# Performance work log

Measured on AMD Instinct MI355X. Metric: run time of the kernel, lower is better.

## Reference

```python
import jax, jax.numpy as jnp
import numpy as np

N = 50000   # num_nodes
R = 8       # num_relations
H = 128     # hidden_l
L = 32      # num_labels
E = 1600000 # num_edges


def setup_inputs() -> dict:
    key = jax.random.key(0)
    ks = jax.random.split(key, 8)
    edge_index = jax.random.randint(ks[0], (2, E), 0, N, dtype=jnp.int64)
    edge_type = jax.random.randint(ks[1], (E,), 0, R, dtype=jnp.int64)
    # layer 1: in_channels = num_nodes (x=None -> one-hot features)
    weight1 = jax.random.normal(ks[2], (R, N, H), dtype=jnp.float32) * 0.02
    root1 = jax.random.normal(ks[3], (N, H), dtype=jnp.float32) * 0.02
    bias1 = jnp.zeros((H,), dtype=jnp.float32)
    # layer 2: hidden -> labels
    weight2 = jax.random.normal(ks[4], (R, H, L), dtype=jnp.float32) * 0.05
    root2 = jax.random.normal(ks[5], (H, L), dtype=jnp.float32) * 0.05
    bias2 = jnp.zeros((L,), dtype=jnp.float32)
    return {"weight1": weight1, "root1": root1, "bias1": bias1,
            "weight2": weight2, "root2": root2, "bias2": bias2,
            "edge_index": edge_index, "edge_type": edge_type}


def _rel_mean_agg(msg, dst, et, num_nodes, num_rel):
    """PyG RGCNConv aggr='mean': mean over incoming edges per (node, relation),
    then sum over relations. msg: [E, F]."""
    seg = dst * num_rel + et  # combined (node, relation) segment id
    sums = jax.ops.segment_sum(msg, seg, num_segments=num_nodes * num_rel)
    cnt = jax.ops.segment_sum(jnp.ones((msg.shape[0],), msg.dtype), seg,
                              num_segments=num_nodes * num_rel)
    mean = sums / jnp.maximum(cnt, 1.0)[:, None]  # zero where count==0
    return mean.reshape(num_nodes, num_rel, -1).sum(axis=1)  # [N, F]


def reference(weight1, root1, bias1, weight2, root2, bias2, edge_index, edge_type):
    src, dst = edge_index[0], edge_index[1]
    # ---- layer 1 (x=None): message = weight1[r, src] row gather ----
    msg1 = weight1[edge_type, src]                      # [E, H]
    x = _rel_mean_agg(msg1, dst, edge_type, N, R) + root1 + bias1
    x = jax.nn.relu(x)
    # ---- layer 2: per-relation matmul then gather ----
    xw = jnp.einsum('nh,rhl->nrl', x, weight2)          # [N, R, L]
    msg2 = xw[src, edge_type]                           # [E, L]
    out = _rel_mean_agg(msg2, dst, edge_type, N, R) + x @ root2 + bias2
    return jax.nn.sigmoid(out)
```

## Files before the change

### kernel.cpp

```cpp
#include <hip/hip_runtime.h>
#include <math.h>

#define NN 50000
#define RR 8
#define HH 128
#define LL 32
#define EE 1600000
#define BW 128
#define NB 391
#define PB 782

#define FMA4(A, V, C) { A.x += (V).x*(C); A.y += (V).y*(C); A.z += (V).z*(C); A.w += (V).w*(C); }

typedef __attribute__((ext_vector_type(8))) short short8_t;
typedef __attribute__((ext_vector_type(4))) float f32x4_t;

__device__ __forceinline__ float bflo(unsigned u) { return __uint_as_float(u << 16); }
__device__ __forceinline__ float bfhi(unsigned u) { return __uint_as_float(u & 0xFFFF0000u); }
__device__ __forceinline__ unsigned bfpk(float a, float b) {
    unsigned ua = __float_as_uint(a), ub = __float_as_uint(b);
    ua = (ua + 0x7FFFu + ((ua >> 16) & 1u)) >> 16;
    ub = (ub + 0x7FFFu + ((ub >> 16) & 1u)) >> 16;
    return ua | (ub << 16);
}
__device__ __forceinline__ unsigned short bf16r(float f) {
    unsigned u = __float_as_uint(f);
    return (unsigned short)((u + 0x7FFFu + ((u >> 16) & 1u)) >> 16);
}

__global__ __launch_bounds__(256) void hist_kernel(const int* __restrict__ ei,
                                                   unsigned* __restrict__ ph) {
    __shared__ unsigned h[NB];
    int blk = blockIdx.x, tid = threadIdx.x;
    for (int i = tid; i < NB; i += 256) h[i] = 0;
    __syncthreads();
    int base = blk * 2048;
    if (blk < PB - 1) {
        const uint4* dp = (const uint4*)(ei + EE + base);
        uint4 d0 = dp[tid], d1 = dp[tid + 256];
        atomicAdd(&h[d0.x >> 7], 1u); atomicAdd(&h[d0.y >> 7], 1u);
        atomicAdd(&h[d0.z >> 7], 1u); atomicAdd(&h[d0.w >> 7], 1u);
        atomicAdd(&h[d1.x >> 7], 1u); atomicAdd(&h[d1.y >> 7], 1u);
        atomicAdd(&h[d1.z >> 7], 1u); atomicAdd(&h[d1.w >> 7], 1u);
    } else {
#pragma unroll
        for (int k = 0; k < 8; ++k) {
            int e = base + k * 256 + tid;
            if (e < EE) atomicAdd(&h[(unsigned)ei[EE + e] >> 7], 1u);
        }
    }
    __syncthreads();
    for (int i = tid; i < NB; i += 256) ph[blk * NB + i] = h[i];
}

__global__ __launch_bounds__(256) void bred_kernel(const unsigned* __restrict__ ph,
                                                   unsigned* __restrict__ pho,
                                                   unsigned* __restrict__ bcnt) {
    __shared__ unsigned s[256];
    int b = blockIdx.x, t = threadIdx.x;
    unsigned v[4];
    unsigned loc = 0;
#pragma unroll
    for (int j = 0; j < 4; ++j) {
        int idx = t * 4 + j;
        v[j] = (idx < PB) ? ph[(size_t)idx * NB + b] : 0;
        loc += v[j];
    }
    s[t] = loc;
    __syncthreads();
    for (int off = 1; off < 256; off <<= 1) {
        unsigned u = (t >= off) ? s[t - off] : 0; __syncthreads();
        if (t >= off) s[t] += u; __syncthreads();
    }
    unsigned run = (t > 0) ? s[t - 1] : 0;
#pragma unroll
    for (int j = 0; j < 4; ++j) {
        int idx = t * 4 + j;
        if (idx < PB) { unsigned c = v[j]; pho[(size_t)b * PB + idx] = run; run += c; }
    }
    if (t == 255) bcnt[b] = s[255];
}

__global__ __launch_bounds__(512) void bscan_kernel(const unsigned* __restrict__ bcnt,
                                                    unsigned* __restrict__ boff,
                                                    unsigned* __restrict__ node_off,
                                                    unsigned* __restrict__ srcr) {
    __shared__ unsigned s[512];
    int t = threadIdx.x;
    unsigned v = (t < NB) ? bcnt[t] : 0;
    s[t] = v; __syncthreads();
    for (int off = 1; off < 512; off <<= 1) {
        unsigned u = (t >= off) ? s[t - off] : 0; __syncthreads();
        if (t >= off) s[t] += u; __syncthreads();
    }
    if (t < NB) boff[t] = s[t] - v;
    if (t == 0) { boff[NB] = EE; node_off[NN] = EE; }
    if (t < 64) srcr[EE + t] = 0;
}

__global__ __launch_bounds__(256) void part_conv(const int* __restrict__ ei,
                                                 const int* __restrict__ et,
                                                 const unsigned* __restrict__ boff,
                                                 const unsigned* __restrict__ pho,
                                                 unsigned* __restrict__ tmp,
                                                 const float4* __restrict__ w1,
                                                 const float* __restrict__ w2,
                                                 uint4* __restrict__ w1b,
                                                 unsigned* __restrict__ wtb) {
    __shared__ unsigned h[NB];
    int b = blockIdx.x, tid = threadIdx.x;
    if (b >= PB) {
        if (b < PB + 25000) {
            size_t t = (size_t)(b - PB) * 256 + tid;
            float4 a = w1[2 * t], c = w1[2 * t + 1];
            uint4 o;
            o.x = bfpk(a.x, a.y); o.y = bfpk(a.z, a.w);
            o.z = bfpk(c.x, c.y); o.w = bfpk(c.z, c.w);
            w1b[t] = o;
        } else {
            int c = tid, r = c >> 5, l = c & 31;
            const float* wp = w2 + (size_t)r * HH * LL + l;
            for (int k = 0; k < HH; k += 2)
                wtb[c * 64 + (k >> 1)] = bfpk(wp[k * LL], wp[(k + 1) * LL]);
        }
        return;
    }
    for (int i = tid; i < NB; i += 256) h[i] = boff[i] + pho[(size_t)i * PB + b];
    __syncthreads();
    int base = b * 2048;
#pragma unroll
    for (int k = 0; k < 8; ++k) {
        int e = base + k * 256 + tid;
        if (e < EE) {
            unsigned sN = (unsigned)ei[e], d = (unsigned)ei[EE + e], r = (unsigned)et[e];
            unsigned p = atomicAdd(&h[d >> 7], 1u);
            tmp[p] = sN | (r << 16) | ((d & 127u) << 19);
        }
    }
}

__global__ __launch_bounds__(256) void finalize_kernel(const unsigned* __restrict__ boff,
                                                       const unsigned* __restrict__ tmp,
                                                       unsigned* __restrict__ node_off,
                                                       float* __restrict__ inv,
                                                       unsigned* __restrict__ srcr) {
    __shared__ unsigned cnt[BW * RR];
    __shared__ unsigned cur[BW];
    __shared__ unsigned excl[BW];
    int b = blockIdx.x, t = threadIdx.x;
    unsigned lo = boff[b], hi = boff[b + 1];
    int nn0 = b * BW;
    int nloc = NN - nn0 < BW ? NN - nn0 : BW;
    for (int i = t; i < BW * RR; i += 256) cnt[i] = 0;
    __syncthreads();
    for (unsigned i = lo + t; i < hi; i += 256) {
        unsigned v = tmp[i];
        atomicAdd(&cnt[((v >> 19) & 127u) * RR + ((v >> 16) & 7u)], 1u);
    }
    __syncthreads();
    unsigned own = 0;
    if (t < BW) {
#pragma unroll
        for (int r = 0; r < RR; ++r) own += cnt[t * RR + r];
        excl[t] = own;
    }
    __syncthreads();
    for (int off = 1; off < BW; off <<= 1) {
        unsigned u = 0;
        if (t < BW && t >= off) u = excl[t - off];
        __syncthreads();
        if (t < BW && t >= off) excl[t] += u;
        __syncthreads();
    }
    if (t < nloc) {
        unsigned o = lo + excl[t] - own;
        node_off[nn0 + t] = o;
        cur[t] = o;
    }
    __syncthreads();
    for (int i = t; i < nloc * RR; i += 256) {
        unsigned c = cnt[i];
        inv[(size_t)nn0 * RR + i] = c ? 1.f / (float)c : 0.f;
    }
    for (unsigned i = lo + t; i < hi; i += 256) {
        unsigned v = tmp[i];
        unsigned p = atomicAdd(&cur[(v >> 19) & 127u], 1u);
        srcr[p] = v & 0x7FFFFu;
    }
}

__global__ __launch_bounds__(256) void l1_gather(const unsigned* __restrict__ node_off,
                                                 const unsigned* __restrict__ srcr,
                                                 const float* __restrict__ inv,
                                                 const uint4* __restrict__ w1b,
                                                 const float* __restrict__ root1,
                                                 const float* __restrict__ bias1,
                                                 uint4* __restrict__ xb) {
    int wid = threadIdx.x >> 6, lane = threadIdx.x & 63;
    int n = blockIdx.x * 4 + wid;
    if (n >= NN) return;
    int q = lane >> 4, ql = lane & 15;
    int beg = node_off[n], end = node_off[n + 1];
    int cnt = end - beg;
    int nfull = cnt >> 4;
    float myinv = inv[n * RR + (lane & 7)];
    float4 a0 = {0.f, 0.f, 0.f, 0.f}, a1 = {0.f, 0.f, 0.f, 0.f};
    int e = beg + q;
    unsigned kp0 = srcr[e], kp1 = srcr[e + 4], kp2 = srcr[e + 8], kp3 = srcr[e + 12];
#define GATH(K, C) {                                                        \
        unsigned ss = (K) & 0xFFFFu, rr = (K) >> 16;                        \
        uint4 v = w1b[((size_t)rr * NN + ss) * 16 + ql];                    \
        a0.x = fmaf(bflo(v.x), (C), a0.x); a0.y = fmaf(bfhi(v.x), (C), a0.y); \
        a0.z = fmaf(bflo(v.y), (C), a0.z); a0.w = fmaf(bfhi(v.y), (C), a0.w); \
        a1.x = fmaf(bflo(v.z), (C), a1.x); a1.y = fmaf(bfhi(v.z), (C), a1.y); \
        a1.z = fmaf(bflo(v.w), (C), a1.z); a1.w = fmaf(bfhi(v.w), (C), a1.w); }
#pragma unroll 1
    for (int it = 0; it < nfull; ++it) {
        unsigned k0 = kp0, k1 = kp1, k2 = kp2, k3 = kp3;
        e += 16;
        kp0 = srcr[e]; kp1 = srcr[e + 4]; kp2 = srcr[e + 8]; kp3 = srcr[e + 12];
        float c0 = __shfl(myinv, (int)(k0 >> 16));
        float c1 = __shfl(myinv, (int)(k1 >> 16));
        float c2 = __shfl(myinv, (int)(k2 >> 16));
        float c3 = __shfl(myinv, (int)(k3 >> 16));
        GATH(k0, c0); GATH(k1, c1); GATH(k2, c2); GATH(k3, c3);
    }
    {
        float c0 = __shfl(myinv, (int)(kp0 >> 16));
        float c1 = __shfl(myinv, (int)(kp1 >> 16));
        float c2 = __shfl(myinv, (int)(kp2 >> 16));
        float c3 = __shfl(myinv, (int)(kp3 >> 16));
        if (e < end)      GATH(kp0, c0);
        if (e + 4 < end)  GATH(kp1, c1);
        if (e + 8 < end)  GATH(kp2, c2);
        if (e + 12 < end) GATH(kp3, c3);
    }
#undef GATH
#define RED(c) { c += __shfl_xor(c, 16); c += __shfl_xor(c, 32); }
    RED(a0.x); RED(a0.y); RED(a0.z); RED(a0.w);
    RED(a1.x); RED(a1.y); RED(a1.z); RED(a1.w);
#undef RED
    if (q == 0) {
        const float4* rt = (const float4*)(root1 + (size_t)n * HH);
        const float4* bs = (const float4*)bias1;
        float4 rA = rt[2 * ql], rB = rt[2 * ql + 1];
        float4 bA = bs[2 * ql], bB = bs[2 * ql + 1];
        float o0 = fmaxf(a0.x + rA.x + bA.x, 0.f);
        float o1 = fmaxf(a0.y + rA.y + bA.y, 0.f);
        float o2 = fmaxf(a0.z + rA.z + bA.z, 0.f);
        float o3 = fmaxf(a0.w + rA.w + bA.w, 0.f);
        float o4 = fmaxf(a1.x + rB.x + bB.x, 0.f);
        float o5 = fmaxf(a1.y + rB.y + bB.y, 0.f);
        float o6 = fmaxf(a1.z + rB.z + bB.z, 0.f);
        float o7 = fmaxf(a1.w + rB.w + bB.w, 0.f);
        uint4 o;
        o.x = bfpk(o0, o1); o.y = bfpk(o2, o3);
        o.z = bfpk(o4, o5); o.w = bfpk(o6, o7);
        xb[(size_t)n * 16 + ql] = o;
    }
}

__global__ __launch_bounds__(256) void xw_mfma(const unsigned* __restrict__ xb,
                                               const unsigned* __restrict__ wtb,
                                               unsigned short* __restrict__ xwb) {
    int tid = threadIdx.x, wid = tid >> 6, l = tid & 63;
    int bn = blockIdx.x >> 2;
    int bc = blockIdx.x & 3;
    int col = bc * 64 + wid * 16 + (l & 15);
    int kq = l >> 4;
    short8_t bfr[4];
    const unsigned* wcol = wtb + col * 64;
#pragma unroll
    for (int ks = 0; ks < 4; ++ks)
        bfr[ks] = *reinterpret_cast<const short8_t*>(wcol + ks * 16 + kq * 4);
    int n0 = bn * 64;
#pragma unroll
    for (int sub = 0; sub < 4; ++sub) {
        int row = n0 + sub * 16 + (l & 15);
        int rc = row < NN ? row : NN - 1;
        const unsigned* xr = xb + (size_t)rc * 64;
        f32x4_t acc = {0.f, 0.f, 0.f, 0.f};
#pragma unroll
        for (int ks = 0; ks < 4; ++ks) {
            short8_t a = *reinterpret_cast<const short8_t*>(xr + ks * 16 + kq * 4);
            acc = __builtin_amdgcn_mfma_f32_16x16x32_bf16(a, bfr[ks], acc, 0, 0, 0);
        }
        int orow0 = n0 + sub * 16 + kq * 4;
#pragma unroll
        for (int j = 0; j < 4; ++j) {
            int orow = orow0 + j;
            if (orow < NN) xwb[(size_t)orow * 256 + col] = bf16r(acc[j]);
        }
    }
}

__global__ __launch_bounds__(256) void l2_gather(const unsigned* __restrict__ node_off,
                                                 const unsigned* __restrict__ srcr,
                                                 const float* __restrict__ inv,
                                                 const uint2* __restrict__ xwb,
                                                 const unsigned* __restrict__ xb,
                                                 const float* __restrict__ root2,
                                                 const float* __restrict__ bias2,
                                                 float* __restrict__ out) {
    int wid = threadIdx.x >> 6, lane = threadIdx.x & 63;
    int n = blockIdx.x * 4 + wid;
    if (n >= NN) return;
    int g = lane >> 3, gl = lane & 7;
    int beg = node_off[n], end = node_off[n + 1];
    int cnt = end - beg;
    int nfull = cnt >> 5;
    float myinv = inv[n * RR + (lane & 7)];
    float4 acc = {0.f, 0.f, 0.f, 0.f};
    int e = beg + g;
    unsigned kp0 = srcr[e], kp1 = srcr[e + 8], kp2 = srcr[e + 16], kp3 = srcr[e + 24];
#define GATH2(K, C) {                                              \
        unsigned ss = (K) & 0xFFFFu, rr = (K) >> 16;               \
        uint2 v = xwb[((size_t)ss * RR + rr) * 8 + gl];            \
        acc.x = fmaf(bflo(v.x), (C), acc.x);                       \
        acc.y = fmaf(bfhi(v.x), (C), acc.y);                       \
        acc.z = fmaf(bflo(v.y), (C), acc.z);                       \
        acc.w = fmaf(bfhi(v.y), (C), acc.w); }
#pragma unroll 1
    for (int it = 0; it < nfull; ++it) {
        unsigned k0 = kp0, k1 = kp1, k2 = kp2, k3 = kp3;
        e += 32;
        kp0 = srcr[e]; kp1 = srcr[e + 8]; kp2 = srcr[e + 16]; kp3 = srcr[e + 24];
        float c0 = __shfl(myinv, (int)(k0 >> 16));
        float c1 = __shfl(myinv, (int)(k1 >> 16));
        float c2 = __shfl(myinv, (int)(k2 >> 16));
        float c3 = __shfl(myinv, (int)(k3 >> 16));
        GATH2(k0, c0); GATH2(k1, c1); GATH2(k2, c2); GATH2(k3, c3);
    }
    {
        float c0 = __shfl(myinv, (int)(kp0 >> 16));
        float c1 = __shfl(myinv, (int)(kp1 >> 16));
        float c2 = __shfl(myinv, (int)(kp2 >> 16));
        float c3 = __shfl(myinv, (int)(kp3 >> 16));
        if (e < end)      GATH2(kp0, c0);
        if (e + 8 < end)  GATH2(kp1, c1);
        if (e + 16 < end) GATH2(kp2, c2);
        if (e + 24 < end) GATH2(kp3, c3);
    }
#undef GATH2
    {
        const uint4* xr = (const uint4*)(xb + (size_t)n * 64);
        uint4 u0 = xr[g * 2], u1 = xr[g * 2 + 1];
        float xv[16] = {bflo(u0.x), bfhi(u0.x), bflo(u0.y), bfhi(u0.y),
                        bflo(u0.z), bfhi(u0.z), bflo(u0.w), bfhi(u0.w),
                        bflo(u1.x), bfhi(u1.x), bflo(u1.y), bfhi(u1.y),
                        bflo(u1.z), bfhi(u1.z), bflo(u1.w), bfhi(u1.w)};
        const float4* rp = (const float4*)root2 + g * 16 * 8 + gl;
#pragma unroll
        for (int i = 0; i < 16; ++i) {
            float4 w = rp[i * 8];
            FMA4(acc, w, xv[i]);
        }
    }
#define RED3(c) { c += __shfl_xor(c, 8); c += __shfl_xor(c, 16); c += __shfl_xor(c, 32); }
    RED3(acc.x); RED3(acc.y); RED3(acc.z); RED3(acc.w);
#undef RED3
    if (lane < 8) {
        float4 b = ((const float4*)bias2)[gl];
        float4 z;
        z.x = 1.f / (1.f + expf(-(acc.x + b.x)));
        z.y = 1.f / (1.f + expf(-(acc.y + b.y)));
        z.z = 1.f / (1.f + expf(-(acc.z + b.z)));
        z.w = 1.f / (1.f + expf(-(acc.w + b.w)));
        ((float4*)(out + (size_t)n * LL))[gl] = z;
    }
}

extern "C" void kernel_launch(void* const* d_in, const int* in_sizes, int n_in,
                              void* d_out, int out_size, void* d_ws, size_t ws_size,
                              hipStream_t stream) {
    const float* w1    = (const float*)d_in[0];
    const float* root1 = (const float*)d_in[1];
    const float* bias1 = (const float*)d_in[2];
    const float* w2    = (const float*)d_in[3];
    const float* root2 = (const float*)d_in[4];
    const float* bias2 = (const float*)d_in[5];
    const int*   ei    = (const int*)d_in[6];
    const int*   et    = (const int*)d_in[7];
    float* out = (float*)d_out;

    float*    inv      = (float*)d_ws;
    unsigned* node_off = (unsigned*)(inv + 400000);
    unsigned* boff     = node_off + 50004;
    unsigned* bcnt     = boff + 400;
    unsigned* ph       = bcnt + 400;
    unsigned* pho      = ph + 305768;
    unsigned* srcr     = pho + 305768;
    unsigned* xb       = srcr + 1600068;
    unsigned* wtb      = xb + 3200000;
    unsigned* w1b      = wtb + 16384;
    unsigned* xwb      = w1b + 25600000;
    unsigned* tmp      = xwb;

    hist_kernel<<<PB, 256, 0, stream>>>(ei, ph);
    bred_kernel<<<NB, 256, 0, stream>>>(ph, pho, bcnt);
    bscan_kernel<<<1, 512, 0, stream>>>(bcnt, boff, node_off, srcr);
    part_conv<<<PB + 25001, 256, 0, stream>>>(ei, et, boff, pho, tmp,
                                              (const float4*)w1, w2, (uint4*)w1b, wtb);
    finalize_kernel<<<NB, 256, 0, stream>>>(boff, tmp, node_off, inv, srcr);
    l1_gather<<<(NN + 3) / 4, 256, 0, stream>>>(node_off, srcr, inv, (const uint4*)w1b,
                                                root1, bias1, (uint4*)xb);
    xw_mfma<<<((NN + 63) / 64) * 4, 256, 0, stream>>>(xb, wtb, (unsigned short*)xwb);
    l2_gather<<<(NN + 3) / 4, 256, 0, stream>>>(node_off, srcr, inv, (const uint2*)xwb,
                                                xb, root2, bias2, out);
}
```

Before: 281.9 us.

## Fuse layer-1 gather with XW MFMA per 64-node block and halve bucket width

Bucket width drops from 128 to 64 nodes, which doubles the number of buckets and changes the histogram, scan and partition kernels to match. The layer-1 gather and the per-relation XW matmul are merged into one 1024-thread kernel: each block gathers 64 nodes, syncs, then runs the MFMA on that same tile. This removes one launch and lets the matmul read its input while it is likely still in cache. In exchange, the larger blocks with a barrier may lose occupancy, waves in a block can be held up by uneven node degrees, and the bigger histogram arrays add scan work.

```diff
diff --git a/kernel.cpp b/kernel.cpp
--- a/kernel.cpp
+++ b/kernel.cpp
@@ -6,8 +6,8 @@
 #define HH 128
 #define LL 32
 #define EE 1600000
-#define BW 128
-#define NB 391
+#define BW 64
+#define NB 782
 #define PB 782
 
 #define FMA4(A, V, C) { A.x += (V).x*(C); A.y += (V).y*(C); A.z += (V).z*(C); A.w += (V).w*(C); }
@@ -38,15 +38,15 @@
     if (blk < PB - 1) {
         const uint4* dp = (const uint4*)(ei + EE + base);
         uint4 d0 = dp[tid], d1 = dp[tid + 256];
-        atomicAdd(&h[d0.x >> 7], 1u); atomicAdd(&h[d0.y >> 7], 1u);
-        atomicAdd(&h[d0.z >> 7], 1u); atomicAdd(&h[d0.w >> 7], 1u);
-        atomicAdd(&h[d1.x >> 7], 1u); atomicAdd(&h[d1.y >> 7], 1u);
-        atomicAdd(&h[d1.z >> 7], 1u); atomicAdd(&h[d1.w >> 7], 1u);
+        atomicAdd(&h[d0.x >> 6], 1u); atomicAdd(&h[d0.y >> 6], 1u);
+        atomicAdd(&h[d0.z >> 6], 1u); atomicAdd(&h[d0.w >> 6], 1u);
+        atomicAdd(&h[d1.x >> 6], 1u); atomicAdd(&h[d1.y >> 6], 1u);
+        atomicAdd(&h[d1.z >> 6], 1u); atomicAdd(&h[d1.w >> 6], 1u);
     } else {
 #pragma unroll
         for (int k = 0; k < 8; ++k) {
             int e = base + k * 256 + tid;
-            if (e < EE) atomicAdd(&h[(unsigned)ei[EE + e] >> 7], 1u);
+            if (e < EE) atomicAdd(&h[(unsigned)ei[EE + e] >> 6], 1u);
         }
     }
     __syncthreads();
@@ -81,19 +81,32 @@
     if (t == 255) bcnt[b] = s[255];
 }
 
-__global__ __launch_bounds__(512) void bscan_kernel(const unsigned* __restrict__ bcnt,
+__global__ __launch_bounds__(256) void bscan_kernel(const unsigned* __restrict__ bcnt,
                                                     unsigned* __restrict__ boff,
                                                     unsigned* __restrict__ node_off,
                                                     unsigned* __restrict__ srcr) {
-    __shared__ unsigned s[512];
+    __shared__ unsigned s[256];
     int t = threadIdx.x;
-    unsigned v = (t < NB) ? bcnt[t] : 0;
-    s[t] = v; __syncthreads();
-    for (int off = 1; off < 512; off <<= 1) {
+    unsigned v[4];
+    unsigned loc = 0;
+#pragma unroll
+    for (int j = 0; j < 4; ++j) {
+        int idx = t * 4 + j;
+        v[j] = (idx < NB) ? bcnt[idx] : 0;
+        loc += v[j];
+    }
+    s[t] = loc;
+    __syncthreads();
+    for (int off = 1; off < 256; off <<= 1) {
         unsigned u = (t >= off) ? s[t - off] : 0; __syncthreads();
         if (t >= off) s[t] += u; __syncthreads();
     }
-    if (t < NB) boff[t] = s[t] - v;
+    unsigned run = (t > 0) ? s[t - 1] : 0;
+#pragma unroll
+    for (int j = 0; j < 4; ++j) {
+        int idx = t * 4 + j;
+        if (idx < NB) { boff[idx] = run; run += v[j]; }
+    }
     if (t == 0) { boff[NB] = EE; node_off[NN] = EE; }
     if (t < 64) srcr[EE + t] = 0;
 }
@@ -133,8 +146,8 @@
         int e = base + k * 256 + tid;
         if (e < EE) {
             unsigned sN = (unsigned)ei[e], d = (unsigned)ei[EE + e], r = (unsigned)et[e];
-            unsigned p = atomicAdd(&h[d >> 7], 1u);
-            tmp[p] = sN | (r << 16) | ((d & 127u) << 19);
+            unsigned p = atomicAdd(&h[d >> 6], 1u);
+            tmp[p] = sN | (r << 16) | ((d & 63u) << 19);
         }
     }
 }
@@ -155,7 +168,7 @@
     __syncthreads();
     for (unsigned i = lo + t; i < hi; i += 256) {
         unsigned v = tmp[i];
-        atomicAdd(&cnt[((v >> 19) & 127u) * RR + ((v >> 16) & 7u)], 1u);
+        atomicAdd(&cnt[((v >> 19) & 63u) * RR + ((v >> 16) & 7u)], 1u);
     }
     __syncthreads();
     unsigned own = 0;
@@ -184,101 +197,99 @@
     }
     for (unsigned i = lo + t; i < hi; i += 256) {
         unsigned v = tmp[i];
-        unsigned p = atomicAdd(&cur[(v >> 19) & 127u], 1u);
+        unsigned p = atomicAdd(&cur[(v >> 19) & 63u], 1u);
         srcr[p] = v & 0x7FFFFu;
     }
 }
 
-__global__ __launch_bounds__(256) void l1_gather(const unsigned* __restrict__ node_off,
-                                                 const unsigned* __restrict__ srcr,
-                                                 const float* __restrict__ inv,
-                                                 const uint4* __restrict__ w1b,
-                                                 const float* __restrict__ root1,
-                                                 const float* __restrict__ bias1,
-                                                 uint4* __restrict__ xb) {
-    int wid = threadIdx.x >> 6, lane = threadIdx.x & 63;
-    int n = blockIdx.x * 4 + wid;
-    if (n >= NN) return;
+__global__ __launch_bounds__(1024, 8) void l1xw_kernel(const unsigned* __restrict__ node_off,
+                                                       const unsigned* __restrict__ srcr,
+                                                       const float* __restrict__ inv,
+                                                       const uint4* __restrict__ w1b,
+                                                       const float* __restrict__ root1,
+                                                       const float* __restrict__ bias1,
+                                                       const unsigned* __restrict__ wtb,
+                                                       uint4* __restrict__ xb,
+                                                       unsigned short* __restrict__ xwb) {
+    int tid = threadIdx.x;
+    int wid = tid >> 6, lane = tid & 63;
+    int n0 = blockIdx.x * 64;
     int q = lane >> 4, ql = lane & 15;
-    int beg = node_off[n], end = node_off[n + 1];
-    int cnt = end - beg;
-    int nfull = cnt >> 4;
-    float myinv = inv[n * RR + (lane & 7)];
-    float4 a0 = {0.f, 0.f, 0.f, 0.f}, a1 = {0.f, 0.f, 0.f, 0.f};
-    int e = beg + q;
-    unsigned kp0 = srcr[e], kp1 = srcr[e + 4], kp2 = srcr[e + 8], kp3 = srcr[e + 12];
+#pragma unroll 1
+    for (int i = 0; i < 4; ++i) {
+        int n = n0 + wid * 4 + i;
+        if (n >= NN) break;
+        int beg = node_off[n], end = node_off[n + 1];
+        int nfull = (end - beg) >> 4;
+        float myinv = inv[n * RR + (lane & 7)];
+        float4 a0 = {0.f, 0.f, 0.f, 0.f}, a1 = {0.f, 0.f, 0.f, 0.f};
+        int e = beg + q;
+        unsigned kp0 = srcr[e], kp1 = srcr[e + 4], kp2 = srcr[e + 8], kp3 = srcr[e + 12];
 #define GATH(K, C) {                                                        \
-        unsigned ss = (K) & 0xFFFFu, rr = (K) >> 16;                        \
-        uint4 v = w1b[((size_t)rr * NN + ss) * 16 + ql];                    \
+        unsigned idx = (((K) >> 16) * (unsigned)NN + ((K) & 0xFFFFu)) * 16u + (unsigned)ql; \
+        uint4 v = w1b[idx];                                                 \
         a0.x = fmaf(bflo(v.x), (C), a0.x); a0.y = fmaf(bfhi(v.x), (C), a0.y); \
         a0.z = fmaf(bflo(v.y), (C), a0.z); a0.w = fmaf(bfhi(v.y), (C), a0.w); \
         a1.x = fmaf(bflo(v.z), (C), a1.x); a1.y = fmaf(bfhi(v.z), (C), a1.y); \
         a1.z = fmaf(bflo(v.w), (C), a1.z); a1.w = fmaf(bfhi(v.w), (C), a1.w); }
 #pragma unroll 1
-    for (int it = 0; it < nfull; ++it) {
-        unsigned k0 = kp0, k1 = kp1, k2 = kp2, k3 = kp3;
-        e += 16;
-        kp0 = srcr[e]; kp1 = srcr[e + 4]; kp2 = srcr[e + 8]; kp3 = srcr[e + 12];
-        float c0 = __shfl(myinv, (int)(k0 >> 16));
-        float c1 = __shfl(myinv, (int)(k1 >> 16));
-        float c2 = __shfl(myinv, (int)(k2 >> 16));
-        float c3 = __shfl(myinv, (int)(k3 >> 16));
-        GATH(k0, c0); GATH(k1, c1); GATH(k2, c2); GATH(k3, c3);
-    }
-    {
-        float c0 = __shfl(myinv, (int)(kp0 >> 16));
-        float c1 = __shfl(myinv, (int)(kp1 >> 16));
-        float c2 = __shfl(myinv, (int)(kp2 >> 16));
-        float c3 = __shfl(myinv, (int)(kp3 >> 16));
-        if (e < end)      GATH(kp0, c0);
-        if (e + 4 < end)  GATH(kp1, c1);
-        if (e + 8 < end)  GATH(kp2, c2);
-        if (e + 12 < end) GATH(kp3, c3);
-    }
+        for (int it = 0; it < nfull; ++it) {
+            unsigned k0 = kp0, k1 = kp1, k2 = kp2, k3 = kp3;
+            e += 16;
+            kp0 = srcr[e]; kp1 = srcr[e + 4]; kp2 = srcr[e + 8]; kp3 = srcr[e + 12];
+            float c0 = __shfl(myinv, (int)(k0 >> 16));
+            float c1 = __shfl(myinv, (int)(k1 >> 16));
+            float c2 = __shfl(myinv, (int)(k2 >> 16));
+            float c3 = __shfl(myinv, (int)(k3 >> 16));
+            GATH(k0, c0); GATH(k1, c1); GATH(k2, c2); GATH(k3, c3);
+        }
+        {
+            float c0 = __shfl(myinv, (int)(kp0 >> 16));
+            float c1 = __shfl(myinv, (int)(kp1 >> 16));
+            float c2 = __shfl(myinv, (int)(kp2 >> 16));
+            float c3 = __shfl(myinv, (int)(kp3 >> 16));
+            if (e < end)      GATH(kp0, c0);
+            if (e + 4 < end)  GATH(kp1, c1);
+            if (e + 8 < end)  GATH(kp2, c2);
+            if (e + 12 < end) GATH(kp3, c3);
+        }
 #undef GATH
 #define RED(c) { c += __shfl_xor(c, 16); c += __shfl_xor(c, 32); }
-    RED(a0.x); RED(a0.y); RED(a0.z); RED(a0.w);
-    RED(a1.x); RED(a1.y); RED(a1.z); RED(a1.w);
+        RED(a0.x); RED(a0.y); RED(a0.z); RED(a0.w);
+        RED(a1.x); RED(a1.y); RED(a1.z); RED(a1.w);
 #undef RED
-    if (q == 0) {
-        const float4* rt = (const float4*)(root1 + (size_t)n * HH);
-        const float4* bs = (const float4*)bias1;
-        float4 rA = rt[2 * ql], rB = rt[2 * ql + 1];
-        float4 bA = bs[2 * ql], bB = bs[2 * ql + 1];
-        float o0 = fmaxf(a0.x + rA.x + bA.x, 0.f);
-        float o1 = fmaxf(a0.y + rA.y + bA.y, 0.f);
-        float o2 = fmaxf(a0.z + rA.z + bA.z, 0.f);
-        float o3 = fmaxf(a0.w + rA.w + bA.w, 0.f);
-        float o4 = fmaxf(a1.x + rB.x + bB.x, 0.f);
-        float o5 = fmaxf(a1.y + rB.y + bB.y, 0.f);
-        float o6 = fmaxf(a1.z + rB.z + bB.z, 0.f);
-        float o7 = fmaxf(a1.w + rB.w + bB.w, 0.f);
-        uint4 o;
-        o.x = bfpk(o0, o1); o.y = bfpk(o2, o3);
-        o.z = bfpk(o4, o5); o.w = bfpk(o6, o7);
-        xb[(size_t)n * 16 + ql] = o;
-    }
-}
-
-__global__ __launch_bounds__(256) void xw_mfma(const unsigned* __restrict__ xb,
-                                               const unsigned* __restrict__ wtb,
-                                               unsigned short* __restrict__ xwb) {
-    int tid = threadIdx.x, wid = tid >> 6, l = tid & 63;
-    int bn = blockIdx.x >> 2;
-    int bc = blockIdx.x & 3;
-    int col = bc * 64 + wid * 16 + (l & 15);
-    int kq = l >> 4;
+        if (q == 0) {
+            const float4* rt = (const float4*)(root1 + (size_t)n * HH);
+            const float4* bs = (const float4*)bias1;
+            float4 rA = rt[2 * ql], rB = rt[2 * ql + 1];
+            float4 bA = bs[2 * ql], bB = bs[2 * ql + 1];
+            float o0 = fmaxf(a0.x + rA.x + bA.x, 0.f);
+            float o1 = fmaxf(a0.y + rA.y + bA.y, 0.f);
+            float o2 = fmaxf(a0.z + rA.z + bA.z, 0.f);
+            float o3 = fmaxf(a0.w + rA.w + bA.w, 0.f);
+            float o4 = fmaxf(a1.x + rB.x + bB.x, 0.f);
+            float o5 = fmaxf(a1.y + rB.y + bB.y, 0.f);
+            float o6 = fmaxf(a1.z + rB.z + bB.z, 0.f);
+            float o7 = fmaxf(a1.w + rB.w + bB.w, 0.f);
+            uint4 o;
+            o.x = bfpk(o0, o1); o.y = bfpk(o2, o3);
+            o.z = bfpk(o4, o5); o.w = bfpk(o6, o7);
+            xb[(size_t)n * 16 + ql] = o;
+        }
+    }
+    __syncthreads();
+    int col = wid * 16 + (lane & 15);
+    int kq = lane >> 4;
     short8_t bfr[4];
     const unsigned* wcol = wtb + col * 64;
 #pragma unroll
     for (int ks = 0; ks < 4; ++ks)
         bfr[ks] = *reinterpret_cast<const short8_t*>(wcol + ks * 16 + kq * 4);
-    int n0 = bn * 64;
 #pragma unroll
     for (int sub = 0; sub < 4; ++sub) {
-        int row = n0 + sub * 16 + (l & 15);
+        int row = n0 + sub * 16 + (lane & 15);
         int rc = row < NN ? row : NN - 1;
-        const unsigned* xr = xb + (size_t)rc * 64;
+        const unsigned* xr = (const unsigned*)xb + (size_t)rc * 64;
         f32x4_t acc = {0.f, 0.f, 0.f, 0.f};
 #pragma unroll
         for (int ks = 0; ks < 4; ++ks) {
@@ -307,15 +318,14 @@
     if (n >= NN) return;
     int g = lane >> 3, gl = lane & 7;
     int beg = node_off[n], end = node_off[n + 1];
-    int cnt = end - beg;
-    int nfull = cnt >> 5;
+    int nfull = (end - beg) >> 5;
     float myinv = inv[n * RR + (lane & 7)];
     float4 acc = {0.f, 0.f, 0.f, 0.f};
     int e = beg + g;
     unsigned kp0 = srcr[e], kp1 = srcr[e + 8], kp2 = srcr[e + 16], kp3 = srcr[e + 24];
 #define GATH2(K, C) {                                              \
-        unsigned ss = (K) & 0xFFFFu, rr = (K) >> 16;               \
-        uint2 v = xwb[((size_t)ss * RR + rr) * 8 + gl];            \
+        unsigned idx = ((((K) >> 16) & 7u) + ((K) & 0xFFFFu) * 8u) * 8u + (unsigned)gl; \
+        uint2 v = xwb[idx];                                        \
         acc.x = fmaf(bflo(v.x), (C), acc.x);                       \
         acc.y = fmaf(bfhi(v.x), (C), acc.y);                       \
         acc.z = fmaf(bflo(v.y), (C), acc.z);                       \
@@ -386,10 +396,10 @@
     float*    inv      = (float*)d_ws;
     unsigned* node_off = (unsigned*)(inv + 400000);
     unsigned* boff     = node_off + 50004;
-    unsigned* bcnt     = boff + 400;
-    unsigned* ph       = bcnt + 400;
-    unsigned* pho      = ph + 305768;
-    unsigned* srcr     = pho + 305768;
+    unsigned* bcnt     = boff + 800;
+    unsigned* ph       = bcnt + 800;
+    unsigned* pho      = ph + 611528;
+    unsigned* srcr     = pho + 611528;
     unsigned* xb       = srcr + 1600068;
     unsigned* wtb      = xb + 3200000;
     unsigned* w1b      = wtb + 16384;
@@ -398,13 +408,13 @@
 
     hist_kernel<<<PB, 256, 0, stream>>>(ei, ph);
     bred_kernel<<<NB, 256, 0, stream>>>(ph, pho, bcnt);
-    bscan_kernel<<<1, 512, 0, stream>>>(bcnt, boff, node_off, srcr);
+    bscan_kernel<<<1, 256, 0, stream>>>(bcnt, boff, node_off, srcr);
     part_conv<<<PB + 25001, 256, 0, stream>>>(ei, et, boff, pho, tmp,
                                               (const float4*)w1, w2, (uint4*)w1b, wtb);
     finalize_kernel<<<NB, 256, 0, stream>>>(boff, tmp, node_off, inv, srcr);
-    l1_gather<<<(NN + 3) / 4, 256, 0, stream>>>(node_off, srcr, inv, (const uint4*)w1b,
-                                                root1, bias1, (uint4*)xb);
-    xw_mfma<<<((NN + 63) / 64) * 4, 256, 0, stream>>>(xb, wtb, (unsigned short*)xwb);
+    l1xw_kernel<<<NB, 1024, 0, stream>>>(node_off, srcr, inv, (const uint4*)w1b,
+                                         root1, bias1, wtb, (uint4*)xb,
+                                         (unsigned short*)xwb);
     l2_gather<<<(NN + 3) / 4, 256, 0, stream>>>(node_off, srcr, inv, (const uint2*)xwb,
                                                 xb, root2, bias2, out);
 }
```

Result: slower. 291.1 us (+3.3%).
